# Kernel optimization log

Measured on AMD Instinct MI355X. Metric: run time of the kernel, lower is better.

Reference implementation:

```python
import jax, jax.numpy as jnp
import numpy as np

SIZE = 1 << 24          # number of leaves (power of two, so bound == SIZE)
BOUND = 1 << 24         # padded power-of-two bound, as in SegmentTree.__init__
LOG2_BOUND = 24         # tree depth; traversal runs exactly this many steps
BATCH = 65536           # number of sampled prefix values


def setup_inputs() -> dict:
    key = jax.random.key(0)
    k1, k2 = jax.random.split(key)
    # leaf priorities must be non-negative (docstring warning for prefix-sum query)
    leaf = jax.random.uniform(k1, (SIZE,), dtype=jnp.float32)
    # fractions in [0,1); scaled by the root sum inside reference
    value_frac = jax.random.uniform(k2, (BATCH,), dtype=jnp.float32)
    return {"leaf": leaf, "value_frac": value_frac}


def _build_tree(leaf):
    """Bottom-up sums: heap layout, tree[1] = root, leaves at tree[BOUND:2*BOUND].
    Equivalent to repeated _setitem parent updates, done level-by-level (vectorized)."""
    levels = [leaf]
    lvl = leaf
    for _ in range(LOG2_BOUND):
        lvl = lvl.reshape(-1, 2).sum(axis=1)  # parent = left + right
        levels.append(lvl)
    # index 0 is an unused dummy slot (heap is 1-indexed)
    return jnp.concatenate([jnp.zeros((1,), leaf.dtype)] + levels[::-1])


def reference(leaf, value_frac):
    tree = _build_tree(leaf)
    # sampled prefix-sum targets in [0, root_sum)
    value = value_frac * tree[1]
    # faithful translation of _get_prefix_sum_idx: root-to-leaf binary descent.
    # The torch while-loop runs exactly log2(bound) iterations (index: 1 -> bound),
    # so a static Python loop is the jit-friendly equivalent.
    index = jnp.ones(value.shape, dtype=jnp.int32)  # 2*BOUND < 2^31, int32 safe
    for _ in range(LOG2_BOUND):
        index = index * 2
        lsons = tree[index]            # left-child subtree sums (gather)
        direct = lsons < value         # go right if left subtree too small
        value = value - lsons * direct
        index = index + direct
    index = index - BOUND              # convert heap position to leaf index
    priorities = leaf[index]           # priority of the sampled leaves
    return index, priorities
```

## Files before the change

kernel.cpp:

```cpp
#include <hip/hip_runtime.h>


#define BATCH_N 65536

#define OFF_ROOT 0
#define OFF_A 16
#define OFF_B 32
#define OFF_C 288
#define OFF_D 4384
#define OFF_E 69920

__device__ __forceinline__ float sum16_exact(float4 A, float4 B, float4 C, float4 D) {
    float n0 = A.x + A.y, n1 = A.z + A.w, n2 = B.x + B.y, n3 = B.z + B.w;
    float n4 = C.x + C.y, n5 = C.z + C.w, n6 = D.x + D.y, n7 = D.z + D.w;
    float m0 = n0 + n1, m1 = n2 + n3, m2 = n4 + n5, m3 = n6 + n7;
    return (m0 + m1) + (m2 + m3);
}

__device__ __forceinline__ float sum16_exact_s(const float* __restrict__ x) {
    float n0 = x[0] + x[1],  n1 = x[2] + x[3],  n2 = x[4] + x[5],  n3 = x[6] + x[7];
    float n4 = x[8] + x[9],  n5 = x[10] + x[11], n6 = x[12] + x[13], n7 = x[14] + x[15];
    float m0 = n0 + n1, m1 = n2 + n3, m2 = n4 + n5, m3 = n6 + n7;
    return (m0 + m1) + (m2 + m3);
}

__global__ __launch_bounds__(256) void build_lo(const float* __restrict__ leaf,
                                                float* __restrict__ ws) {
    __shared__ float smE[256];
    __shared__ float smD[16];
    const int t = threadIdx.x;
    const int b = blockIdx.x;
    const size_t gid = (size_t)b * 256 + t;
    const float4* q = reinterpret_cast<const float4*>(leaf) + gid * 4;
    float4 A = q[0], Bv = q[1], Cv = q[2], Dv = q[3];
    float e = sum16_exact(A, Bv, Cv, Dv);
    ws[OFF_E + gid] = e;
    smE[t] = e;
    __syncthreads();
    if (t < 16) {
        float d = sum16_exact_s(&smE[16 * t]);
        ws[OFF_D + (size_t)b * 16 + t] = d;
        smD[t] = d;
    }
    __syncthreads();
    if (t == 0) {
        ws[OFF_C + b] = sum16_exact_s(smD);
    }
}

__global__ __launch_bounds__(256) void build_top(float* __restrict__ ws) {
    __shared__ float smB[256];
    __shared__ float smA[16];
    const int t = threadIdx.x;
    const float4* q = reinterpret_cast<const float4*>(ws + OFF_C) + (size_t)t * 4;
    float4 A = q[0], Bv = q[1], Cv = q[2], Dv = q[3];
    float bnode = sum16_exact(A, Bv, Cv, Dv);
    ws[OFF_B + t] = bnode;
    smB[t] = bnode;
    __syncthreads();
    if (t < 16) {
        float anode = sum16_exact_s(&smB[16 * t]);
        ws[OFF_A + t] = anode;
        smA[t] = anode;
    }
    __syncthreads();
    if (t == 0) {
        ws[OFF_ROOT] = sum16_exact_s(smA);
    }
}

__device__ __forceinline__ void step16(const float* __restrict__ base, int& p, float& v,
                                       float& picked) {
    const float4* q = reinterpret_cast<const float4*>(base + (size_t)p * 16);
    float4 A = q[0], B = q[1], C = q[2], D = q[3];
    float n0 = A.x + A.y, n2 = B.x + B.y, n4 = C.x + C.y, n6 = D.x + D.y;
    float m0 = n0 + (A.z + A.w);
    float m2 = n4 + (C.z + C.w);
    float t0 = m0 + (n2 + (B.z + B.w));

    int ia = t0 < v;  if (ia) v -= t0;
    float mm = ia ? m2 : m0;
    int ib = mm < v;  if (ib) v -= mm;
    float nn = ia ? (ib ? n6 : n4) : (ib ? n2 : n0);
    int ic = nn < v;  if (ic) v -= nn;
    float se0 = ia ? C.x : A.x, se1 = ia ? C.z : A.z;
    float se2 = ia ? D.x : B.x, se3 = ia ? D.z : B.z;
    float so0 = ia ? C.y : A.y, so1 = ia ? C.w : A.w;
    float so2 = ia ? D.y : B.y, so3 = ia ? D.w : B.w;
    float ce = ic ? (ib ? se3 : se1) : (ib ? se2 : se0);
    float co = ic ? (ib ? so3 : so1) : (ib ? so2 : so0);
    int id = ce < v;  if (id) v -= ce;
    picked = id ? co : ce;
    p = p * 16 + ia * 8 + ib * 4 + ic * 2 + id;
}

__global__ __launch_bounds__(256) void descend(const float* __restrict__ leaf,
                                               const float* __restrict__ frac,
                                               const float* __restrict__ ws,
                                               float* __restrict__ out) {
    const int tid = blockIdx.x * 256 + threadIdx.x;
    float v = frac[tid] * ws[OFF_ROOT];
    int p = 0;
    float picked = 0.0f;
    step16(ws + OFF_A, p, v, picked);
    step16(ws + OFF_B, p, v, picked);
    step16(ws + OFF_C, p, v, picked);
    step16(ws + OFF_D, p, v, picked);
    step16(ws + OFF_E, p, v, picked);
    step16(leaf,       p, v, picked);
    out[tid] = (float)p;
    out[BATCH_N + tid] = picked;
}

extern "C" void kernel_launch(void* const* d_in, const int* in_sizes, int n_in,
                              void* d_out, int out_size, void* d_ws, size_t ws_size,
                              hipStream_t stream) {
    const float* leaf = (const float*)d_in[0];
    const float* frac = (const float*)d_in[1];
    float* out = (float*)d_out;
    float* ws  = (float*)d_ws;

    hipLaunchKernelGGL(build_lo,  dim3(4096), dim3(256), 0, stream, leaf, ws);
    hipLaunchKernelGGL(build_top, dim3(1),    dim3(256), 0, stream, ws);
    hipLaunchKernelGGL(descend,   dim3(256),  dim3(256), 0, stream, leaf, frac, ws, out);
}
```

Measured before the change: 97.85 us.

## Fuse top tree build into descend kernel with swizzled LDS levels

```diff
diff --git a/kernel.cpp b/kernel.cpp
--- a/kernel.cpp
+++ b/kernel.cpp
@@ -3,12 +3,16 @@
 
 #define BATCH_N 65536
 
-#define OFF_ROOT 0
-#define OFF_A 16
-#define OFF_B 32
 #define OFF_C 288
 #define OFF_D 4384
 #define OFF_E 69920
+
+__device__ __forceinline__ int swz_f4(int s) {
+    return (s & ~3) | ((s & 3) ^ ((s >> 2) & 3));
+}
+__device__ __forceinline__ int swz_sc(int i) {
+    return swz_f4(i >> 2) * 4 + (i & 3);
+}
 
 __device__ __forceinline__ float sum16_exact(float4 A, float4 B, float4 C, float4 D) {
     float n0 = A.x + A.y, n1 = A.z + A.w, n2 = B.x + B.y, n3 = B.z + B.w;
@@ -30,12 +34,27 @@
     __shared__ float smD[16];
     const int t = threadIdx.x;
     const int b = blockIdx.x;
-    const size_t gid = (size_t)b * 256 + t;
-    const float4* q = reinterpret_cast<const float4*>(leaf) + gid * 4;
-    float4 A = q[0], Bv = q[1], Cv = q[2], Dv = q[3];
-    float e = sum16_exact(A, Bv, Cv, Dv);
-    ws[OFF_E + gid] = e;
-    smE[t] = e;
+    const float4* base = reinterpret_cast<const float4*>(leaf) + (size_t)b * 1024;
+    float4 r0 = base[t];
+    float4 r1 = base[256 + t];
+    float4 r2 = base[512 + t];
+    float4 r3 = base[768 + t];
+    float m0 = (r0.x + r0.y) + (r0.z + r0.w);
+    float m1 = (r1.x + r1.y) + (r1.z + r1.w);
+    float m2 = (r2.x + r2.y) + (r2.z + r2.w);
+    float m3 = (r3.x + r3.y) + (r3.z + r3.w);
+    float e0 = m0 + __shfl_xor(m0, 1); e0 = e0 + __shfl_xor(e0, 2);
+    float e1 = m1 + __shfl_xor(m1, 1); e1 = e1 + __shfl_xor(e1, 2);
+    float e2 = m2 + __shfl_xor(m2, 1); e2 = e2 + __shfl_xor(e2, 2);
+    float e3 = m3 + __shfl_xor(m3, 1); e3 = e3 + __shfl_xor(e3, 2);
+    float* outE = ws + OFF_E + (size_t)b * 256;
+    if ((t & 3) == 0) {
+        const int g = t >> 2;
+        outE[g]       = e0;  smE[g]       = e0;
+        outE[64 + g]  = e1;  smE[64 + g]  = e1;
+        outE[128 + g] = e2;  smE[128 + g] = e2;
+        outE[192 + g] = e3;  smE[192 + g] = e3;
+    }
     __syncthreads();
     if (t < 16) {
         float d = sum16_exact_s(&smE[16 * t]);
@@ -48,31 +67,8 @@
     }
 }
 
-__global__ __launch_bounds__(256) void build_top(float* __restrict__ ws) {
-    __shared__ float smB[256];
-    __shared__ float smA[16];
-    const int t = threadIdx.x;
-    const float4* q = reinterpret_cast<const float4*>(ws + OFF_C) + (size_t)t * 4;
-    float4 A = q[0], Bv = q[1], Cv = q[2], Dv = q[3];
-    float bnode = sum16_exact(A, Bv, Cv, Dv);
-    ws[OFF_B + t] = bnode;
-    smB[t] = bnode;
-    __syncthreads();
-    if (t < 16) {
-        float anode = sum16_exact_s(&smB[16 * t]);
-        ws[OFF_A + t] = anode;
-        smA[t] = anode;
-    }
-    __syncthreads();
-    if (t == 0) {
-        ws[OFF_ROOT] = sum16_exact_s(smA);
-    }
-}
-
-__device__ __forceinline__ void step16(const float* __restrict__ base, int& p, float& v,
-                                       float& picked) {
-    const float4* q = reinterpret_cast<const float4*>(base + (size_t)p * 16);
-    float4 A = q[0], B = q[1], C = q[2], D = q[3];
+__device__ __forceinline__ void step16_core(float4 A, float4 B, float4 C, float4 D,
+                                            int& p, float& v, float& picked) {
     float n0 = A.x + A.y, n2 = B.x + B.y, n4 = C.x + C.y, n6 = D.x + D.y;
     float m0 = n0 + (A.z + A.w);
     float m2 = n4 + (C.z + C.w);
@@ -94,20 +90,84 @@
     p = p * 16 + ia * 8 + ib * 4 + ic * 2 + id;
 }
 
+__device__ __forceinline__ void step16_g(const float* __restrict__ base, int& p,
+                                         float& v, float& picked) {
+    const float4* q = reinterpret_cast<const float4*>(base) + (size_t)p * 4;
+    step16_core(q[0], q[1], q[2], q[3], p, v, picked);
+}
+
+__device__ __forceinline__ void step16_lds(const float* base, int& p,
+                                           float& v, float& picked) {
+    const float4* q = reinterpret_cast<const float4*>(base);
+    const int b4 = p * 4, px = p & 3;
+    float4 A = q[b4 + (0 ^ px)];
+    float4 B = q[b4 + (1 ^ px)];
+    float4 C = q[b4 + (2 ^ px)];
+    float4 D = q[b4 + (3 ^ px)];
+    step16_core(A, B, C, D, p, v, picked);
+}
+
 __global__ __launch_bounds__(256) void descend(const float* __restrict__ leaf,
                                                const float* __restrict__ frac,
                                                const float* __restrict__ ws,
                                                float* __restrict__ out) {
-    const int tid = blockIdx.x * 256 + threadIdx.x;
-    float v = frac[tid] * ws[OFF_ROOT];
+    __shared__ float sC[4096];
+    __shared__ float sB[256];
+    __shared__ float sA[16];
+    __shared__ float sRoot;
+    const int t = threadIdx.x;
+
+    const float4* Cg = reinterpret_cast<const float4*>(ws + OFF_C);
+    float4* sC4 = reinterpret_cast<float4*>(sC);
+    float4 r0 = Cg[t];
+    float4 r1 = Cg[256 + t];
+    float4 r2 = Cg[512 + t];
+    float4 r3 = Cg[768 + t];
+    sC4[swz_f4(t)]       = r0;
+    sC4[swz_f4(256 + t)] = r1;
+    sC4[swz_f4(512 + t)] = r2;
+    sC4[swz_f4(768 + t)] = r3;
+    float m0 = (r0.x + r0.y) + (r0.z + r0.w);
+    float m1 = (r1.x + r1.y) + (r1.z + r1.w);
+    float m2 = (r2.x + r2.y) + (r2.z + r2.w);
+    float m3 = (r3.x + r3.y) + (r3.z + r3.w);
+    float e0 = m0 + __shfl_xor(m0, 1); e0 = e0 + __shfl_xor(e0, 2);
+    float e1 = m1 + __shfl_xor(m1, 1); e1 = e1 + __shfl_xor(e1, 2);
+    float e2 = m2 + __shfl_xor(m2, 1); e2 = e2 + __shfl_xor(e2, 2);
+    float e3 = m3 + __shfl_xor(m3, 1); e3 = e3 + __shfl_xor(e3, 2);
+    if ((t & 3) == 0) {
+        const int g = t >> 2;
+        sB[swz_sc(g)]       = e0;
+        sB[swz_sc(64 + g)]  = e1;
+        sB[swz_sc(128 + g)] = e2;
+        sB[swz_sc(192 + g)] = e3;
+    }
+    __syncthreads();
+    if (t < 16) {
+        const float4* sB4 = reinterpret_cast<const float4*>(sB);
+        const int b4 = t * 4, px = t & 3;
+        float4 A_ = sB4[b4 + (0 ^ px)];
+        float4 B_ = sB4[b4 + (1 ^ px)];
+        float4 C_ = sB4[b4 + (2 ^ px)];
+        float4 D_ = sB4[b4 + (3 ^ px)];
+        sA[t] = sum16_exact(A_, B_, C_, D_);
+    }
+    __syncthreads();
+    if (t == 0) {
+        sRoot = sum16_exact_s(sA);
+    }
+    __syncthreads();
+
+    const int tid = blockIdx.x * 256 + t;
+    float v = frac[tid] * sRoot;
     int p = 0;
     float picked = 0.0f;
-    step16(ws + OFF_A, p, v, picked);
-    step16(ws + OFF_B, p, v, picked);
-    step16(ws + OFF_C, p, v, picked);
-    step16(ws + OFF_D, p, v, picked);
-    step16(ws + OFF_E, p, v, picked);
-    step16(leaf,       p, v, picked);
+    step16_lds(sA, p, v, picked);
+    step16_lds(sB, p, v, picked);
+    step16_lds(sC, p, v, picked);
+    step16_g(ws + OFF_D, p, v, picked);
+    step16_g(ws + OFF_E, p, v, picked);
+    step16_g(leaf,       p, v, picked);
     out[tid] = (float)p;
     out[BATCH_N + tid] = picked;
 }
@@ -120,7 +180,6 @@
     float* out = (float*)d_out;
     float* ws  = (float*)d_ws;
 
-    hipLaunchKernelGGL(build_lo,  dim3(4096), dim3(256), 0, stream, leaf, ws);
-    hipLaunchKernelGGL(build_top, dim3(1),    dim3(256), 0, stream, ws);
-    hipLaunchKernelGGL(descend,   dim3(256),  dim3(256), 0, stream, leaf, frac, ws, out);
+    hipLaunchKernelGGL(build_lo, dim3(4096), dim3(256), 0, stream, leaf, ws);
+    hipLaunchKernelGGL(descend,  dim3(256),  dim3(256), 0, stream, leaf, frac, ws, out);
 }
```

Measured after the change: 95.99 us. No clear change (-1.9%).
